# Kernel optimization log

Hardware: AMD Instinct MI355X
Metric: run time of the kernel (lower is better)

## Reference

```python
import jax, jax.numpy as jnp
import numpy as np

N_GROUPS = 8
N_TOPK_GROUP = 4
TOPK = 8
ROUTED_SCALE = 2.5


def setup_inputs() -> dict:
    key = jax.random.key(0)
    k1, k2, k3 = jax.random.split(key, 3)
    T, D, E = 8192, 7168, 256
    x = jax.random.normal(k1, (T, D), dtype=jnp.float32)
    weight = jax.random.normal(k2, (E, D), dtype=jnp.float32) * 0.02
    bias = jax.random.normal(k3, (E,), dtype=jnp.float32) * 0.02
    return {"x": x, "weight": weight, "bias": bias}


def reference(x, weight, bias):
    T = x.shape[0]
    # gate projection + sigmoid -> routing scores [T, E]
    scores = jax.nn.sigmoid(jnp.einsum("td,ed->te", x, weight))
    original_scores = scores
    s = scores + bias
    # grouped top-k routing: [T, G, E/G]
    sg = s.reshape(T, N_GROUPS, -1)
    # group score = sum of top-2 expert scores within each group
    group_scores = jax.lax.top_k(sg, 2)[0].sum(axis=-1)        # [T, G]
    _, gidx = jax.lax.top_k(group_scores, N_TOPK_GROUP)        # [T, n_topk_group]
    keep = jnp.zeros((T, N_GROUPS), dtype=bool)
    keep = keep.at[jnp.arange(T)[:, None], gidx].set(True)
    sg = jnp.where(keep[:, :, None], sg, -jnp.inf)
    s = sg.reshape(T, -1)
    # per-token top-k experts over surviving groups
    _, indices = jax.lax.top_k(s, TOPK)                        # [T, topk]
    weights = jnp.take_along_axis(original_scores, indices, axis=1)
    weights = weights / weights.sum(axis=-1, keepdims=True) * ROUTED_SCALE
    return weights.astype(x.dtype), indices
```

## Files before the change

kernel.cpp:

```cpp
#include <hip/hip_runtime.h>
#include <hip/hip_bf16.h>
#include <math.h>


typedef _Float16 f16x8 __attribute__((ext_vector_type(8)));
typedef float    f32x4 __attribute__((ext_vector_type(4)));

__device__ __forceinline__ void glds16(const void* g, void* l) {
  __builtin_amdgcn_global_load_lds(
      (const __attribute__((address_space(1))) void*)g,
      (__attribute__((address_space(3))) void*)l, 16, 0, 0);
}

__device__ __forceinline__ unsigned short f2h(float f) {
  _Float16 h = (_Float16)f;
  return __builtin_bit_cast(unsigned short, h);
}
__device__ __forceinline__ float h2f(unsigned short b) {
  return (float)__builtin_bit_cast(_Float16, b);
}

__device__ __forceinline__ int swz(int gi, int row) {
  return gi ^ (row & 3) ^ ((row >> 2) & 3);
}

__global__ __launch_bounds__(256) void convert_w(
    const float* __restrict__ W,
    unsigned short* __restrict__ Whi, unsigned short* __restrict__ Wlo)
{
  const int e = blockIdx.x;
  const int t = threadIdx.x;
  if (t >= 224) return;
  const float* src = W + (size_t)e * 7168 + t * 32;
  const size_t tbase = (size_t)t * 8192 + (size_t)e * 32;
  #pragma unroll
  for (int g = 0; g < 4; ++g) {
    unsigned int hw[4], lw[4];
    #pragma unroll
    for (int p = 0; p < 4; ++p) {
      float f0 = src[g * 8 + 2 * p] * 64.0f;
      float f1 = src[g * 8 + 2 * p + 1] * 64.0f;
      unsigned short h0 = f2h(f0), h1 = f2h(f1);
      unsigned short l0 = f2h((f0 - h2f(h0)) * 2048.0f);
      unsigned short l1 = f2h((f1 - h2f(h1)) * 2048.0f);
      hw[p] = (unsigned)h0 | ((unsigned)h1 << 16);
      lw[p] = (unsigned)l0 | ((unsigned)l1 << 16);
    }
    const size_t base = tbase + (size_t)(swz(g, e) * 8);
    *(uint4*)(Whi + base) = make_uint4(hw[0], hw[1], hw[2], hw[3]);
    *(uint4*)(Wlo + base) = make_uint4(lw[0], lw[1], lw[2], lw[3]);
  }
}

#define BUF_SZ   49152
#define O_ALO    8192
#define O_BH     16384
#define O_BL     32768

__global__ __launch_bounds__(512, 2) void gate_gemm(
    const float* __restrict__ X,
    const unsigned short* __restrict__ Whi,
    const unsigned short* __restrict__ Wlo,
    float* __restrict__ Spart, int D, int TILES, int KS)
{
  __shared__ char lds[147456];

  const int bid = blockIdx.x;
  const int ks = bid % KS;
  const int bm = bid / KS;
  const int tid = threadIdx.x, lane = tid & 63, wid = tid >> 6;
  const int wm = wid >> 2, wn = wid & 3;
  const int TM = bm * 128;
  const int k0base = ks * TILES * 32;

  const int srow = tid >> 2, sg = tid & 3;
  const float* xsrc = X + (size_t)(TM + srow) * D + k0base + sg * 8;
  const int aw = srow * 64 + swz(sg, srow) * 16;

  const unsigned short* wh_tile = Whi + (size_t)(ks * TILES) * 8192;
  const unsigned short* wl_tile = Wlo + (size_t)(ks * TILES) * 8192;

  f32x4 acc1[4][4], acc2[4][4];
  #pragma unroll
  for (int m = 0; m < 4; ++m)
    #pragma unroll
    for (int n = 0; n < 4; ++n) { acc1[m][n] = (f32x4)0.0f; acc2[m][n] = (f32x4)0.0f; }

  int aro[4], bro[4];
  const int gi = lane >> 4;
  #pragma unroll
  for (int m = 0; m < 4; ++m) {
    const int row = wm * 64 + m * 16 + (lane & 15);
    aro[m] = row * 64 + swz(gi, row) * 16;
  }
  #pragma unroll
  for (int n = 0; n < 4; ++n) {
    const int row = wn * 64 + n * 16 + (lane & 15);
    bro[n] = row * 64 + swz(gi, row) * 16;
  }

  float4 pa0, pa1, pb0, pb1;
  {
    float4 a0 = *(const float4*)(xsrc);
    float4 a1 = *(const float4*)(xsrc + 4);
    #pragma unroll
    for (int i = 0; i < 2; ++i) {
      const int c = wid * 2 + i;
      glds16(wh_tile + c * 512 + lane * 8, lds + O_BH + c * 1024);
      glds16(wl_tile + c * 512 + lane * 8, lds + O_BL + c * 1024);
    }
    if (TILES > 1) {
      #pragma unroll
      for (int i = 0; i < 2; ++i) {
        const int c = wid * 2 + i;
        glds16(wh_tile + 8192 + c * 512 + lane * 8, lds + BUF_SZ + O_BH + c * 1024);
        glds16(wl_tile + 8192 + c * 512 + lane * 8, lds + BUF_SZ + O_BL + c * 1024);
      }
    }
    __builtin_amdgcn_sched_barrier(0);
    const int s1 = (TILES > 1) ? 1 : 0;
    pa0 = *(const float4*)(xsrc + (size_t)s1 * 32);
    pa1 = *(const float4*)(xsrc + (size_t)s1 * 32 + 4);
    __builtin_amdgcn_sched_barrier(0);
    float ff[8] = {a0.x, a0.y, a0.z, a0.w, a1.x, a1.y, a1.z, a1.w};
    unsigned int hw[4], lw[4];
    #pragma unroll
    for (int q = 0; q < 4; ++q) {
      float f0 = ff[2 * q], f1 = ff[2 * q + 1];
      unsigned short h0 = f2h(f0), h1 = f2h(f1);
      unsigned short l0 = f2h((f0 - h2f(h0)) * 2048.0f);
      unsigned short l1 = f2h((f1 - h2f(h1)) * 2048.0f);
      hw[q] = (unsigned)h0 | ((unsigned)h1 << 16);
      lw[q] = (unsigned)l0 | ((unsigned)l1 << 16);
    }
    *(uint4*)(lds + aw)         = make_uint4(hw[0], hw[1], hw[2], hw[3]);
    *(uint4*)(lds + O_ALO + aw) = make_uint4(lw[0], lw[1], lw[2], lw[3]);
    __builtin_amdgcn_sched_barrier(0);
  }
  asm volatile("s_waitcnt vmcnt(6) lgkmcnt(0)" ::: "memory");
  __builtin_amdgcn_sched_barrier(0);
  __builtin_amdgcn_s_barrier();

  for (int s = 0; s < TILES; ++s) {
    char* base_c  = lds + (s % 3) * BUF_SZ;
    char* base_n1 = lds + ((s + 1) % 3) * BUF_SZ;
    char* base_n2 = lds + ((s + 2) % 3) * BUF_SZ;

    if (s + 2 < TILES) {
      const unsigned short* wh = wh_tile + (size_t)(s + 2) * 8192;
      const unsigned short* wl = wl_tile + (size_t)(s + 2) * 8192;
      #pragma unroll
      for (int i = 0; i < 2; ++i) {
        const int c = wid * 2 + i;
        glds16(wh + c * 512 + lane * 8, base_n2 + O_BH + c * 1024);
        glds16(wl + c * 512 + lane * 8, base_n2 + O_BL + c * 1024);
      }
    }
    __builtin_amdgcn_sched_barrier(0);

    {
      int sn = s + 2; if (sn > TILES - 1) sn = TILES - 1;
      pb0 = *(const float4*)(xsrc + (size_t)sn * 32);
      pb1 = *(const float4*)(xsrc + (size_t)sn * 32 + 4);
    }
    __builtin_amdgcn_sched_barrier(0);

    {
      const char* Ahi = base_c;         const char* Alo = base_c + O_ALO;
      const char* Bh  = base_c + O_BH;  const char* Bl  = base_c + O_BL;
      f16x8 ah[4], al[4], bh[4], bl[4];
      #pragma unroll
      for (int m = 0; m < 4; ++m) {
        ah[m] = *(const f16x8*)(Ahi + aro[m]);
        al[m] = *(const f16x8*)(Alo + aro[m]);
      }
      #pragma unroll
      for (int n = 0; n < 4; ++n) {
        bh[n] = *(const f16x8*)(Bh + bro[n]);
        bl[n] = *(const f16x8*)(Bl + bro[n]);
      }
      __builtin_amdgcn_s_setprio(1);
      #pragma unroll
      for (int m = 0; m < 4; ++m)
        #pragma unroll
        for (int n = 0; n < 4; ++n) {
          acc1[m][n] = __builtin_amdgcn_mfma_f32_16x16x32_f16(ah[m], bh[n], acc1[m][n], 0, 0, 0);
          acc2[m][n] = __builtin_amdgcn_mfma_f32_16x16x32_f16(ah[m], bl[n], acc2[m][n], 0, 0, 0);
          acc2[m][n] = __builtin_amdgcn_mfma_f32_16x16x32_f16(al[m], bh[n], acc2[m][n], 0, 0, 0);
        }
      __builtin_amdgcn_s_setprio(0);
    }

    if (s + 1 < TILES) {
      float ff[8] = {pa0.x, pa0.y, pa0.z, pa0.w, pa1.x, pa1.y, pa1.z, pa1.w};
      unsigned int hw[4], lw[4];
      #pragma unroll
      for (int q = 0; q < 4; ++q) {
        float f0 = ff[2 * q], f1 = ff[2 * q + 1];
        unsigned short h0 = f2h(f0), h1 = f2h(f1);
        unsigned short l0 = f2h((f0 - h2f(h0)) * 2048.0f);
        unsigned short l1 = f2h((f1 - h2f(h1)) * 2048.0f);
        hw[q] = (unsigned)h0 | ((unsigned)h1 << 16);
        lw[q] = (unsigned)l0 | ((unsigned)l1 << 16);
      }
      *(uint4*)(base_n1 + aw)         = make_uint4(hw[0], hw[1], hw[2], hw[3]);
      *(uint4*)(base_n1 + O_ALO + aw) = make_uint4(lw[0], lw[1], lw[2], lw[3]);
    }
    pa0 = pb0; pa1 = pb1;

    asm volatile("s_waitcnt vmcnt(6) lgkmcnt(0)" ::: "memory");
    __builtin_amdgcn_sched_barrier(0);
    __builtin_amdgcn_s_barrier();
  }

  float* Sp = Spart + (size_t)ks * 8192 * 256;
  #pragma unroll
  for (int m = 0; m < 4; ++m)
    #pragma unroll
    for (int n = 0; n < 4; ++n)
      #pragma unroll
      for (int r = 0; r < 4; ++r) {
        const int t = TM + wm * 64 + m * 16 + (lane >> 4) * 4 + r;
        const int e = wn * 64 + n * 16 + (lane & 15);
        Sp[(size_t)t * 256 + e] =
            (acc1[m][n][r] + acc2[m][n][r] * (1.0f / 2048.0f)) * (1.0f / 64.0f);
      }
}

__global__ __launch_bounds__(256) void gate_routing(
    const float* __restrict__ Spart, int KS,
    const float* __restrict__ bias,
    float* __restrict__ outw, float* __restrict__ outi, int T)
{
  const int lane = threadIdx.x & 63;
  const int wave = threadIdx.x >> 6;
  const int t = blockIdx.x * 4 + wave;
  if (t >= T) return;

  double l[4] = {0.0, 0.0, 0.0, 0.0};
  for (int ks = 0; ks < KS; ++ks) {
    float4 p = *(const float4*)(Spart + (size_t)ks * T * 256
                                + (size_t)t * 256 + lane * 4);
    l[0] += (double)p.x; l[1] += (double)p.y;
    l[2] += (double)p.z; l[3] += (double)p.w;
  }

  float4 bi = *(const float4*)(bias + lane * 4);
  float orig[4], s[4];
  #pragma unroll
  for (int u = 0; u < 4; ++u)
    orig[u] = 1.0f / (1.0f + expf(-(float)l[u]));
  s[0] = orig[0] + bi.x; s[1] = orig[1] + bi.y;
  s[2] = orig[2] + bi.z; s[3] = orig[3] + bi.w;

  float m1 = -INFINITY, m2 = -INFINITY;
  #pragma unroll
  for (int u = 0; u < 4; ++u) {
    float v = s[u];
    if (v > m1) { m2 = m1; m1 = v; }
    else if (v > m2) { m2 = v; }
  }
  #pragma unroll
  for (int off = 1; off < 8; off <<= 1) {
    float o1 = __shfl_xor(m1, off, 64);
    float o2 = __shfl_xor(m2, off, 64);
    if (o1 > m1) { m2 = fmaxf(m1, o2); m1 = o1; }
    else         { m2 = fmaxf(m2, o1); }
  }
  const float gscore = m1 + m2;

  const int g = lane >> 3;
  int rank = 0;
  #pragma unroll
  for (int j = 0; j < 8; ++j) {
    float gs = __shfl(gscore, j * 8, 64);
    rank += (gs > gscore || (gs == gscore && j < g)) ? 1 : 0;
  }
  if (rank >= 4) { s[0] = s[1] = s[2] = s[3] = -INFINITY; }

  float wsum = 0.0f, sel_w = 0.0f;
  int sel_i = 0;
  #pragma unroll
  for (int it = 0; it < 8; ++it) {
    float bv = s[0]; int bu = 0;
    #pragma unroll
    for (int u = 1; u < 4; ++u)
      if (s[u] > bv) { bv = s[u]; bu = u; }
    float v = bv;
    int ix = lane * 4 + bu;
    float og = orig[bu];
    #pragma unroll
    for (int off = 1; off < 64; off <<= 1) {
      float ov  = __shfl_xor(v,  off, 64);
      int   oix = __shfl_xor(ix, off, 64);
      float oog = __shfl_xor(og, off, 64);
      if (ov > v || (ov == v && oix < ix)) { v = ov; ix = oix; og = oog; }
    }
    if (lane == it) { sel_w = og; sel_i = ix; }
    wsum += og;
    if ((ix >> 2) == lane) s[ix & 3] = -INFINITY;
  }

  if (lane < 8) {
    outw[(size_t)t * 8 + lane] = sel_w / wsum * 2.5f;
    outi[(size_t)t * 8 + lane] = (float)sel_i;
  }
}

extern "C" void kernel_launch(void* const* d_in, const int* in_sizes, int n_in,
                              void* d_out, int out_size, void* d_ws, size_t ws_size,
                              hipStream_t stream) {
  const float* x = (const float*)d_in[0];
  const float* w = (const float*)d_in[1];
  const float* b = (const float*)d_in[2];
  const int E = in_sizes[2];
  const int D = in_sizes[1] / E;
  const int T = in_sizes[0] / D;

  unsigned short* Whi = (unsigned short*)d_ws;
  unsigned short* Wlo = (unsigned short*)((char*)d_ws + (4u << 20));
  float* Spart = (float*)((char*)d_ws + (8u << 20));

  const size_t per_part = (size_t)T * E * 4;
  int KS = 2;
  if (ws_size >= (8u << 20) + 4 * per_part) KS = 4;
  const int TILES = D / (32 * KS);

  float* outw = (float*)d_out;
  float* outi = outw + (size_t)T * 8;

  convert_w<<<E, 256, 0, stream>>>(w, Whi, Wlo);
  gate_gemm<<<KS * (T / 128), 512, 0, stream>>>(x, Whi, Wlo, Spart, D, TILES, KS);
  gate_routing<<<(T + 3) / 4, 256, 0, stream>>>(Spart, KS, b, outw, outi, T);
}
```

Baseline: 119.5 us.

## Fuse routing into GEMM epilogue via last-arriving split-K block counter

Removes the separate routing kernel launch by having the last of the KS split-K blocks for each 128-token row tile, detected with an atomic counter, perform the reduction and grouped top-k routing for those tokens. Counters are zeroed inside the weight-conversion kernel. KS is now fixed at 4 with no workspace-size check. The tail work runs on only one block per row tile with 16 tokens per wave, which may serialize routing compared with the wide standalone launch, but it saves a launch and lets reading the partials overlap with other blocks' GEMM work.

Result: slower. 312.9 us (+162.0%).

```diff
diff --git a/kernel.cpp b/kernel.cpp
--- a/kernel.cpp
+++ b/kernel.cpp
@@ -26,11 +26,16 @@
 
 __global__ __launch_bounds__(256) void convert_w(
     const float* __restrict__ W,
-    unsigned short* __restrict__ Whi, unsigned short* __restrict__ Wlo)
+    unsigned short* __restrict__ Whi, unsigned short* __restrict__ Wlo,
+    int* __restrict__ cnt)
 {
   const int e = blockIdx.x;
   const int t = threadIdx.x;
-  if (t >= 224) return;
+  if (t >= 224) {
+    const int idx = e * 32 + (t - 224);
+    if (e < 2) cnt[idx] = 0;
+    return;
+  }
   const float* src = W + (size_t)e * 7168 + t * 32;
   const size_t tbase = (size_t)t * 8192 + (size_t)e * 32;
   #pragma unroll
@@ -61,9 +66,13 @@
     const float* __restrict__ X,
     const unsigned short* __restrict__ Whi,
     const unsigned short* __restrict__ Wlo,
-    float* __restrict__ Spart, int D, int TILES, int KS)
+    float* __restrict__ Spart, int D, int TILES, int KS,
+    const float* __restrict__ bias,
+    float* __restrict__ outw, float* __restrict__ outi,
+    int* __restrict__ cnt, int T)
 {
   __shared__ char lds[147456];
+  __shared__ int done_s;
 
   const int bid = blockIdx.x;
   const int ks = bid % KS;
@@ -213,7 +222,7 @@
     __builtin_amdgcn_s_barrier();
   }
 
-  float* Sp = Spart + (size_t)ks * 8192 * 256;
+  float* Sp = Spart + (size_t)ks * T * 256;
   #pragma unroll
   for (int m = 0; m < 4; ++m)
     #pragma unroll
@@ -225,85 +234,84 @@
         Sp[(size_t)t * 256 + e] =
             (acc1[m][n][r] + acc2[m][n][r] * (1.0f / 2048.0f)) * (1.0f / 64.0f);
       }
-}
-
-__global__ __launch_bounds__(256) void gate_routing(
-    const float* __restrict__ Spart, int KS,
-    const float* __restrict__ bias,
-    float* __restrict__ outw, float* __restrict__ outi, int T)
-{
-  const int lane = threadIdx.x & 63;
-  const int wave = threadIdx.x >> 6;
-  const int t = blockIdx.x * 4 + wave;
-  if (t >= T) return;
-
-  double l[4] = {0.0, 0.0, 0.0, 0.0};
-  for (int ks = 0; ks < KS; ++ks) {
-    float4 p = *(const float4*)(Spart + (size_t)ks * T * 256
-                                + (size_t)t * 256 + lane * 4);
-    l[0] += (double)p.x; l[1] += (double)p.y;
-    l[2] += (double)p.z; l[3] += (double)p.w;
-  }
-
-  float4 bi = *(const float4*)(bias + lane * 4);
-  float orig[4], s[4];
-  #pragma unroll
-  for (int u = 0; u < 4; ++u)
-    orig[u] = 1.0f / (1.0f + expf(-(float)l[u]));
-  s[0] = orig[0] + bi.x; s[1] = orig[1] + bi.y;
-  s[2] = orig[2] + bi.z; s[3] = orig[3] + bi.w;
-
-  float m1 = -INFINITY, m2 = -INFINITY;
-  #pragma unroll
-  for (int u = 0; u < 4; ++u) {
-    float v = s[u];
-    if (v > m1) { m2 = m1; m1 = v; }
-    else if (v > m2) { m2 = v; }
-  }
-  #pragma unroll
-  for (int off = 1; off < 8; off <<= 1) {
-    float o1 = __shfl_xor(m1, off, 64);
-    float o2 = __shfl_xor(m2, off, 64);
-    if (o1 > m1) { m2 = fmaxf(m1, o2); m1 = o1; }
-    else         { m2 = fmaxf(m2, o1); }
-  }
-  const float gscore = m1 + m2;
-
-  const int g = lane >> 3;
-  int rank = 0;
-  #pragma unroll
-  for (int j = 0; j < 8; ++j) {
-    float gs = __shfl(gscore, j * 8, 64);
-    rank += (gs > gscore || (gs == gscore && j < g)) ? 1 : 0;
-  }
-  if (rank >= 4) { s[0] = s[1] = s[2] = s[3] = -INFINITY; }
-
-  float wsum = 0.0f, sel_w = 0.0f;
-  int sel_i = 0;
-  #pragma unroll
-  for (int it = 0; it < 8; ++it) {
-    float bv = s[0]; int bu = 0;
-    #pragma unroll
-    for (int u = 1; u < 4; ++u)
-      if (s[u] > bv) { bv = s[u]; bu = u; }
-    float v = bv;
-    int ix = lane * 4 + bu;
-    float og = orig[bu];
-    #pragma unroll
-    for (int off = 1; off < 64; off <<= 1) {
-      float ov  = __shfl_xor(v,  off, 64);
-      int   oix = __shfl_xor(ix, off, 64);
-      float oog = __shfl_xor(og, off, 64);
-      if (ov > v || (ov == v && oix < ix)) { v = ov; ix = oix; og = oog; }
-    }
-    if (lane == it) { sel_w = og; sel_i = ix; }
-    wsum += og;
-    if ((ix >> 2) == lane) s[ix & 3] = -INFINITY;
-  }
-
-  if (lane < 8) {
-    outw[(size_t)t * 8 + lane] = sel_w / wsum * 2.5f;
-    outi[(size_t)t * 8 + lane] = (float)sel_i;
+
+  __threadfence();
+  if (tid == 0) done_s = atomicAdd(&cnt[bm], 1);
+  __syncthreads();
+  if (done_s != KS - 1) return;
+  __threadfence();
+
+  for (int i = 0; i < 16; ++i) {
+    const int t = TM + wid * 16 + i;
+
+    double l[4] = {0.0, 0.0, 0.0, 0.0};
+    for (int k = 0; k < KS; ++k) {
+      float4 p = *(const float4*)(Spart + (size_t)k * T * 256
+                                  + (size_t)t * 256 + lane * 4);
+      l[0] += (double)p.x; l[1] += (double)p.y;
+      l[2] += (double)p.z; l[3] += (double)p.w;
+    }
+
+    float4 bi = *(const float4*)(bias + lane * 4);
+    float orig[4], s[4];
+    #pragma unroll
+    for (int u = 0; u < 4; ++u)
+      orig[u] = 1.0f / (1.0f + expf(-(float)l[u]));
+    s[0] = orig[0] + bi.x; s[1] = orig[1] + bi.y;
+    s[2] = orig[2] + bi.z; s[3] = orig[3] + bi.w;
+
+    float m1 = -INFINITY, m2 = -INFINITY;
+    #pragma unroll
+    for (int u = 0; u < 4; ++u) {
+      float v = s[u];
+      if (v > m1) { m2 = m1; m1 = v; }
+      else if (v > m2) { m2 = v; }
+    }
+    #pragma unroll
+    for (int off = 1; off < 8; off <<= 1) {
+      float o1 = __shfl_xor(m1, off, 64);
+      float o2 = __shfl_xor(m2, off, 64);
+      if (o1 > m1) { m2 = fmaxf(m1, o2); m1 = o1; }
+      else         { m2 = fmaxf(m2, o1); }
+    }
+    const float gscore = m1 + m2;
+
+    const int g = lane >> 3;
+    int rank = 0;
+    #pragma unroll
+    for (int j = 0; j < 8; ++j) {
+      float gs = __shfl(gscore, j * 8, 64);
+      rank += (gs > gscore || (gs == gscore && j < g)) ? 1 : 0;
+    }
+    if (rank >= 4) { s[0] = s[1] = s[2] = s[3] = -INFINITY; }
+
+    float wsum = 0.0f, sel_w = 0.0f;
+    int sel_i = 0;
+    #pragma unroll
+    for (int it = 0; it < 8; ++it) {
+      float bv = s[0]; int bu = 0;
+      #pragma unroll
+      for (int u = 1; u < 4; ++u)
+        if (s[u] > bv) { bv = s[u]; bu = u; }
+      float v = bv;
+      int ix = lane * 4 + bu;
+      float og = orig[bu];
+      #pragma unroll
+      for (int off = 1; off < 64; off <<= 1) {
+        float ov  = __shfl_xor(v,  off, 64);
+        int   oix = __shfl_xor(ix, off, 64);
+        float oog = __shfl_xor(og, off, 64);
+        if (ov > v || (ov == v && oix < ix)) { v = ov; ix = oix; og = oog; }
+      }
+      if (lane == it) { sel_w = og; sel_i = ix; }
+      wsum += og;
+      if ((ix >> 2) == lane) s[ix & 3] = -INFINITY;
+    }
+
+    if (lane < 8) {
+      outw[(size_t)t * 8 + lane] = sel_w / wsum * 2.5f;
+      outi[(size_t)t * 8 + lane] = (float)sel_i;
+    }
   }
 }
 
@@ -322,14 +330,14 @@
   float* Spart = (float*)((char*)d_ws + (8u << 20));
 
   const size_t per_part = (size_t)T * E * 4;
-  int KS = 2;
-  if (ws_size >= (8u << 20) + 4 * per_part) KS = 4;
+  const int KS = 4;
   const int TILES = D / (32 * KS);
+  int* cnt = (int*)((char*)d_ws + (8u << 20) + (size_t)KS * per_part);
 
   float* outw = (float*)d_out;
   float* outi = outw + (size_t)T * 8;
 
-  convert_w<<<E, 256, 0, stream>>>(w, Whi, Wlo);
-  gate_gemm<<<KS * (T / 128), 512, 0, stream>>>(x, Whi, Wlo, Spart, D, TILES, KS);
-  gate_routing<<<(T + 3) / 4, 256, 0, stream>>>(Spart, KS, b, outw, outi, T);
-}
+  convert_w<<<E, 256, 0, stream>>>(w, Whi, Wlo, cnt);
+  gate_gemm<<<KS * (T / 128), 512, 0, stream>>>(
+      x, Whi, Wlo, Spart, D, TILES, KS, b, outw, outi, cnt, T);
+}
```
